# Optimization experiments

Hardware: AMD Instinct MI355X
Metric: run time of the kernel (lower is better)

## Reference

```python
import jax, jax.numpy as jnp
import numpy as np

N = 50000   # nodes
E = 800000  # edges (no self loops; conv adds them)
F = 64      # in_channels == out_channels
P = 6       # pos dim (pos_nn MLP input = 6)
H = 64      # hidden width of pos_nn / attn_nn


def _mlp(x, W1, b1, W2, b2):
    # PyG MLP([a, 64, b], norm=None, plain_last=False): ReLU after both layers
    return jax.nn.relu(jax.nn.relu(x @ W1 + b1) @ W2 + b2)


def setup_inputs() -> dict:
    key = jax.random.key(0)
    ks = jax.random.split(key, 16)

    def w(k, shape, fan_in):
        return jax.random.normal(k, shape, jnp.float32) / np.sqrt(fan_in)

    src = jax.random.randint(ks[0], (E,), 0, N)
    dst = jax.random.randint(ks[1], (E,), 0, N)
    src = jnp.where(src == dst, (src + 1) % N, src)  # no pre-existing self loops
    edge_index = jnp.stack([src, dst]).astype(jnp.int32)

    return dict(
        x=jax.random.normal(ks[2], (N, F), jnp.float32),
        pos=jax.random.normal(ks[3], (N, P), jnp.float32),
        edge_index=edge_index,
        W_in=w(ks[4], (F, F), F), b_in=jnp.zeros((F,), jnp.float32),
        W_out=w(ks[5], (F, F), F), b_out=jnp.zeros((F,), jnp.float32),
        W_lin=w(ks[6], (F, F), F),   # conv value proj, bias=False
        W_src=w(ks[7], (F, F), F),   # lin_src, bias=False
        W_dst=w(ks[8], (F, F), F),   # lin_dst, bias=False
        Wp1=w(ks[9], (P, H), P), bp1=jnp.zeros((H,), jnp.float32),
        Wp2=w(ks[10], (H, F), H), bp2=jnp.zeros((F,), jnp.float32),
        Wa1=w(ks[11], (F, H), F), ba1=jnp.zeros((H,), jnp.float32),
        Wa2=w(ks[12], (H, F), H), ba2=jnp.zeros((F,), jnp.float32),
    )


def reference(x, pos, edge_index, W_in, b_in, W_out, b_out, W_lin, W_src, W_dst,
              Wp1, bp1, Wp2, bp2, Wa1, ba1, Wa2, ba2):
    residual = jax.lax.stop_gradient(x)  # residual = x.clone().detach()
    h = jax.nn.relu(x @ W_in + b_in)

    # PointTransformerConv
    a_src = h @ W_src
    a_dst = h @ W_dst
    v = h @ W_lin

    loop = jnp.arange(N, dtype=edge_index.dtype)  # add_self_loops=True
    src = jnp.concatenate([edge_index[0], loop])
    dst = jnp.concatenate([edge_index[1], loop])

    delta = _mlp(pos[dst] - pos[src], Wp1, bp1, Wp2, bp2)        # pos_nn(pos_i - pos_j)
    alpha = _mlp(a_dst[dst] - a_src[src] + delta, Wa1, ba1, Wa2, ba2)

    # scatter-softmax over destination neighborhoods (per channel)
    m = jax.ops.segment_max(alpha, dst, num_segments=N)
    e = jnp.exp(alpha - m[dst])
    s = jax.ops.segment_sum(e, dst, num_segments=N)
    wgt = e / (s[dst] + 1e-16)

    msg = wgt * (v[src] + delta)
    out = jax.ops.segment_sum(msg, dst, num_segments=N)

    out = jax.nn.relu(out @ W_out + b_out)
    return out + residual
```

## Files before the change

### kernel.cpp

```cpp
#include <hip/hip_runtime.h>

#define NN 50000
#define NE 800000
#define ETOT (NE + NN)
#define NB ((NN + 255) / 256)

typedef _Float16 f16;
typedef _Float16 v8h __attribute__((ext_vector_type(8)));
typedef float v4f __attribute__((ext_vector_type(4)));

__device__ __forceinline__ float bcast(float v, int lane) {
  return __int_as_float(__builtin_amdgcn_readlane(__float_as_int(v), lane));
}

__device__ __forceinline__ int fr_off(int kb, int nb, int q, int p) {
  return (((nb * 2 + kb) * 4 + q) * 16 + p) * 8;
}


__global__ __launch_bounds__(256) void k_setup(
    const float* __restrict__ W_in, const float* __restrict__ W_src,
    const float* __restrict__ W_dst, const float* __restrict__ W_lin,
    const float* __restrict__ W_out, const float* __restrict__ Wp2,
    const float* __restrict__ Wa1, const float* __restrict__ Wa2,
    const float* __restrict__ Wp1, f16* __restrict__ FR,
    const int* __restrict__ edst, int* __restrict__ deg) {
  const int t = blockIdx.x * 256 + threadIdx.x;
  if (t < NE) atomicAdd(&deg[edst[t]], 1);
  if (t < 8 * 4096) {
    const float* Ws[8] = {W_in, W_src, W_dst, W_lin, W_out, Wp2, Wa1, Wa2};
    const int m = t >> 12, idx = t & 4095;
    const int i = idx & 7, p = (idx >> 3) & 15, q = (idx >> 7) & 3;
    const int kb = (idx >> 9) & 1, nb = (idx >> 10) & 3;
    FR[t] = (f16)Ws[m][(kb * 32 + q * 8 + i) * 64 + nb * 16 + p];
  } else if (t < 8 * 4096 + 2048) {
    const int idx = t - 8 * 4096;
    const int i = idx & 7, p = (idx >> 3) & 15, q = (idx >> 7) & 3, nb = idx >> 9;
    const int k = q * 8 + i;
    FR[t] = (k < 6) ? (f16)Wp1[k * 64 + nb * 16 + p] : (f16)0.f;
  }
}


__global__ __launch_bounds__(256) void k_scan1(const int* __restrict__ deg,
                                               int* __restrict__ bsum) {
  __shared__ int ws[4];
  const int t = threadIdx.x, b = blockIdx.x;
  const int i = b * 256 + t;
  int s = (i < NN) ? (deg[i] + 1) : 0;
#pragma unroll
  for (int d = 1; d < 64; d <<= 1) s += __shfl_xor(s, d, 64);
  if ((t & 63) == 0) ws[t >> 6] = s;
  __syncthreads();
  if (t == 0) bsum[b] = ws[0] + ws[1] + ws[2] + ws[3];
}

__global__ __launch_bounds__(256) void k_scan2(const int* __restrict__ bsum,
                                               int* __restrict__ bpre,
                                               int* __restrict__ offsets) {
  __shared__ int ws[4];
  const int t = threadIdx.x, lane = t & 63, w = t >> 6;
  int v = (t < NB) ? bsum[t] : 0;
  int x = v;
#pragma unroll
  for (int d = 1; d < 64; d <<= 1) {
    int y = __shfl_up(x, d, 64);
    if (lane >= d) x += y;
  }
  if (lane == 63) ws[w] = x;
  __syncthreads();
  if (t == 0) {
    int c = 0;
#pragma unroll
    for (int j = 0; j < 4; ++j) { int tmp = ws[j]; ws[j] = c; c += tmp; }
    offsets[NN] = c;
  }
  __syncthreads();
  if (t < NB) bpre[t] = ws[w] + x - v;
}

__global__ __launch_bounds__(256) void k_scan3(
    const int* __restrict__ deg, const int* __restrict__ bpre,
    int* __restrict__ offsets, int* __restrict__ ssrc, int* __restrict__ cursor) {
  __shared__ int ws[4], wpre[4];
  const int t = threadIdx.x, b = blockIdx.x, lane = t & 63, w = t >> 6;
  const int i = b * 256 + t;
  int v = (i < NN) ? (deg[i] + 1) : 0;
  int x = v;
#pragma unroll
  for (int d = 1; d < 64; d <<= 1) {
    int y = __shfl_up(x, d, 64);
    if (lane >= d) x += y;
  }
  if (lane == 63) ws[w] = x;
  __syncthreads();
  if (t == 0) {
    int c = 0;
#pragma unroll
    for (int j = 0; j < 4; ++j) { wpre[j] = c; c += ws[j]; }
  }
  __syncthreads();
  if (i < NN) {
    const int off = bpre[b] + wpre[w] + x - v;
    offsets[i] = off;
    ssrc[off] = i;
    cursor[i] = off + 1;
  }
}

__global__ void k_scatter(const int* __restrict__ src, const int* __restrict__ dst,
                          int* __restrict__ cursor, int* __restrict__ ssrc) {
  int e = blockIdx.x * 256 + threadIdx.x;
  if (e < NE) {
    int p = atomicAdd(&cursor[dst[e]], 1);
    ssrc[p] = src[e];
  }
}


__global__ __launch_bounds__(256, 2) void k_node(
    const float* __restrict__ x, const float* __restrict__ pos,
    const float* __restrict__ b_in, const f16* __restrict__ FR,
    f16* __restrict__ adsth, f16* __restrict__ vh,
    f16* __restrict__ asrch, f16* __restrict__ Qh) {
  __shared__ f16 lds[4][16 * 72];
  const int lane = threadIdx.x & 63, w = threadIdx.x >> 6;
  const int q = lane >> 4, p = lane & 15;
  const int base = (blockIdx.x * 4 + w) * 16;
  if (base >= NN) return;
  const f16* FWin = FR;
  const f16* FWsrc = FR + 1 * 4096;
  const f16* FWdst = FR + 2 * 4096;
  const f16* FWlin = FR + 3 * 4096;
  const f16* FWp1 = FR + 8 * 4096;

  v8h xa[2];
#pragma unroll
  for (int kb = 0; kb < 2; ++kb) {
    const float4 f0 = *(const float4*)(x + (base + p) * 64 + kb * 32 + q * 8);
    const float4 f1 = *(const float4*)(x + (base + p) * 64 + kb * 32 + q * 8 + 4);
    v8h a;
    a[0] = (f16)f0.x; a[1] = (f16)f0.y; a[2] = (f16)f0.z; a[3] = (f16)f0.w;
    a[4] = (f16)f1.x; a[5] = (f16)f1.y; a[6] = (f16)f1.z; a[7] = (f16)f1.w;
    xa[kb] = a;
  }
#pragma unroll
  for (int nb = 0; nb < 4; ++nb) {
    v4f c = {0.f, 0.f, 0.f, 0.f};
    c = __builtin_amdgcn_mfma_f32_16x16x32_f16(xa[0], *(const v8h*)&FWin[fr_off(0, nb, q, p)], c, 0, 0, 0);
    c = __builtin_amdgcn_mfma_f32_16x16x32_f16(xa[1], *(const v8h*)&FWin[fr_off(1, nb, q, p)], c, 0, 0, 0);
    const float bi = b_in[p + 16 * nb];
#pragma unroll
    for (int r = 0; r < 4; ++r)
      lds[w][(q * 4 + r) * 72 + p + 16 * nb] = (f16)fmaxf(c[r] + bi, 0.f);
  }
  v8h hA[2];
#pragma unroll
  for (int kb = 0; kb < 2; ++kb)
    hA[kb] = *(const v8h*)&lds[w][p * 72 + kb * 32 + q * 8];

#pragma unroll
  for (int nb = 0; nb < 4; ++nb) {
    v4f c = {0.f, 0.f, 0.f, 0.f};
    c = __builtin_amdgcn_mfma_f32_16x16x32_f16(hA[0], *(const v8h*)&FWsrc[fr_off(0, nb, q, p)], c, 0, 0, 0);
    c = __builtin_amdgcn_mfma_f32_16x16x32_f16(hA[1], *(const v8h*)&FWsrc[fr_off(1, nb, q, p)], c, 0, 0, 0);
#pragma unroll
    for (int r = 0; r < 4; ++r)
      asrch[(base + q * 4 + r) * 64 + p + 16 * nb] = (f16)c[r];
  }
#pragma unroll
  for (int nb = 0; nb < 4; ++nb) {
    v4f c = {0.f, 0.f, 0.f, 0.f};
    c = __builtin_amdgcn_mfma_f32_16x16x32_f16(hA[0], *(const v8h*)&FWdst[fr_off(0, nb, q, p)], c, 0, 0, 0);
    c = __builtin_amdgcn_mfma_f32_16x16x32_f16(hA[1], *(const v8h*)&FWdst[fr_off(1, nb, q, p)], c, 0, 0, 0);
#pragma unroll
    for (int r = 0; r < 4; ++r)
      adsth[(base + q * 4 + r) * 64 + p + 16 * nb] = (f16)c[r];
  }
#pragma unroll
  for (int nb = 0; nb < 4; ++nb) {
    v4f c = {0.f, 0.f, 0.f, 0.f};
    c = __builtin_amdgcn_mfma_f32_16x16x32_f16(hA[0], *(const v8h*)&FWlin[fr_off(0, nb, q, p)], c, 0, 0, 0);
    c = __builtin_amdgcn_mfma_f32_16x16x32_f16(hA[1], *(const v8h*)&FWlin[fr_off(1, nb, q, p)], c, 0, 0, 0);
#pragma unroll
    for (int r = 0; r < 4; ++r)
      vh[(base + q * 4 + r) * 64 + p + 16 * nb] = (f16)c[r];
  }
  v8h pa;
#pragma unroll
  for (int i = 0; i < 8; ++i) {
    const int k = q * 8 + i;
    pa[i] = (k < 6) ? (f16)pos[(base + p) * 6 + k] : (f16)0.f;
  }
#pragma unroll
  for (int nb = 0; nb < 4; ++nb) {
    const v8h b = *(const v8h*)&FWp1[(((nb * 4 + q) * 16) + p) * 8];
    v4f c = {0.f, 0.f, 0.f, 0.f};
    c = __builtin_amdgcn_mfma_f32_16x16x32_f16(pa, b, c, 0, 0, 0);
#pragma unroll
    for (int r = 0; r < 4; ++r)
      Qh[(base + q * 4 + r) * 64 + p + 16 * nb] = (f16)c[r];
  }
}


__global__ __launch_bounds__(512, 4) void k_conv(
    const f16* __restrict__ Qh, const float* __restrict__ bp1,
    const f16* __restrict__ FRconv,
    const float* __restrict__ bp2, const float* __restrict__ ba1,
    const float* __restrict__ ba2,
    const f16* __restrict__ asrch, const f16* __restrict__ adsth,
    const f16* __restrict__ vh,
    const int* __restrict__ offsets, const int* __restrict__ ssrc,
    const float* __restrict__ W_out, const float* __restrict__ b_out,
    const float* __restrict__ x, float* __restrict__ out) {
  __shared__ f16 wfr[12288];
  __shared__ f16 tbufD[8][16 * 72];
  __shared__ f16 tbufH[8][16 * 72];
  __shared__ f16 stashQ[8][64];
  __shared__ f16 stashA[8][64];
  __shared__ float bias[192];
  const int t = threadIdx.x;
#pragma unroll
  for (int it = 0; it < 3; ++it)
    *(uint4*)&wfr[(it * 512 + t) * 8] = *(const uint4*)&FRconv[(it * 512 + t) * 8];
  if (t < 192) bias[t] = (t < 64) ? bp2[t] : (t < 128 ? ba1[t - 64] : ba2[t - 128]);

  const int lane = t & 63, w = t >> 6;
  const int q = lane >> 4, p = lane & 15;
  const int n = blockIdx.x * 8 + w;

  stashQ[w][lane] = (f16)((float)Qh[n * 64 + lane] + bp1[lane]);
  stashA[w][lane] = adsth[n * 64 + lane];
  __syncthreads();

  const int e0 = __builtin_amdgcn_readfirstlane(offsets[n]);
  const int e1 = __builtin_amdgcn_readfirstlane(offsets[n + 1]);
  const int cnt = e1 - e0;

  float s_[4], ac_[4];
#pragma unroll
  for (int nb = 0; nb < 4; ++nb) { s_[nb] = 0.f; ac_[nb] = 0.f; }

  for (int cb = 0; cb < cnt; cb += 16) {
    const int jA = ssrc[e0 + min(cb + p, cnt - 1)];
    v8h qj[2], aj[2], vA[2];
#pragma unroll
    for (int kb = 0; kb < 2; ++kb) {
      qj[kb] = *(const v8h*)(Qh + jA * 64 + kb * 32 + q * 8);
      aj[kb] = *(const v8h*)(asrch + jA * 64 + kb * 32 + q * 8);
      vA[kb] = *(const v8h*)(vh + jA * 64 + kb * 32 + q * 8);
    }
    v8h uA[2];
#pragma unroll
    for (int kb = 0; kb < 2; ++kb) {
      const v8h qi = *(const v8h*)&stashQ[w][kb * 32 + q * 8];
      v8h a;
#pragma unroll
      for (int i = 0; i < 8; ++i) {
        const f16 d = qi[i] - qj[kb][i];
        a[i] = d > (f16)0 ? d : (f16)0;
      }
      uA[kb] = a;
    }
    unsigned z0;
    asm volatile("v_mov_b32 %0, 0" : "=v"(z0));
#pragma unroll
    for (int nb = 0; nb < 4; ++nb) {
      v4f c = {0.f, 0.f, 0.f, 0.f};
      c = __builtin_amdgcn_mfma_f32_16x16x32_f16(uA[0], *(const v8h*)&wfr[z0 + fr_off(0, nb, q, p)], c, 0, 0, 0);
      c = __builtin_amdgcn_mfma_f32_16x16x32_f16(uA[1], *(const v8h*)&wfr[z0 + fr_off(1, nb, q, p)], c, 0, 0, 0);
      const float bp2c = bias[p + 16 * nb];
#pragma unroll
      for (int r = 0; r < 4; ++r)
        tbufD[w][(q * 4 + r) * 72 + p + 16 * nb] = (f16)fmaxf(c[r] + bp2c, 0.f);
    }
#pragma unroll
    for (int kb = 0; kb < 2; ++kb) {
      const v8h adc = *(const v8h*)&stashA[w][kb * 32 + q * 8];
      const v8h dj = *(const v8h*)&tbufD[w][p * 72 + kb * 32 + q * 8];
      uA[kb] = (adc - aj[kb]) + dj;
    }
    unsigned z1;
    asm volatile("v_mov_b32 %0, 4096" : "=v"(z1));
#pragma unroll
    for (int nb = 0; nb < 4; ++nb) {
      v4f c = {0.f, 0.f, 0.f, 0.f};
      c = __builtin_amdgcn_mfma_f32_16x16x32_f16(uA[0], *(const v8h*)&wfr[z1 + fr_off(0, nb, q, p)], c, 0, 0, 0);
      c = __builtin_amdgcn_mfma_f32_16x16x32_f16(uA[1], *(const v8h*)&wfr[z1 + fr_off(1, nb, q, p)], c, 0, 0, 0);
      const float ba1c = bias[64 + p + 16 * nb];
#pragma unroll
      for (int r = 0; r < 4; ++r)
        tbufH[w][(q * 4 + r) * 72 + p + 16 * nb] = (f16)fmaxf(c[r] + ba1c, 0.f);
    }
#pragma unroll
    for (int kb = 0; kb < 2; ++kb)
      uA[kb] = *(const v8h*)&tbufH[w][p * 72 + kb * 32 + q * 8];
#pragma unroll
    for (int kb = 0; kb < 2; ++kb)
      *(v8h*)&tbufH[w][p * 72 + kb * 32 + q * 8] = vA[kb];
    unsigned z2;
    asm volatile("v_mov_b32 %0, 8192" : "=v"(z2));
#pragma unroll
    for (int nb = 0; nb < 4; ++nb) {
      v4f c = {0.f, 0.f, 0.f, 0.f};
      c = __builtin_amdgcn_mfma_f32_16x16x32_f16(uA[0], *(const v8h*)&wfr[z2 + fr_off(0, nb, q, p)], c, 0, 0, 0);
      c = __builtin_amdgcn_mfma_f32_16x16x32_f16(uA[1], *(const v8h*)&wfr[z2 + fr_off(1, nb, q, p)], c, 0, 0, 0);
      const float ba2c = bias[128 + p + 16 * nb];
#pragma unroll
      for (int r = 0; r < 4; ++r) {
        const bool ok = (cb + q * 4 + r) < cnt;
        const float al = ok ? fmaxf(c[r] + ba2c, 0.f) : -3.0e38f;
        const float wv = __expf(al);
        const float vj = (float)tbufH[w][(q * 4 + r) * 72 + p + 16 * nb];
        const float dC = (float)tbufD[w][(q * 4 + r) * 72 + p + 16 * nb];
        s_[nb] += wv;
        ac_[nb] = fmaf(wv, vj + dC, ac_[nb]);
      }
    }
  }
#pragma unroll
  for (int st = 16; st <= 32; st <<= 1) {
#pragma unroll
    for (int nb = 0; nb < 4; ++nb) {
      s_[nb] += __shfl_xor(s_[nb], st, 64);
      ac_[nb] += __shfl_xor(ac_[nb], st, 64);
    }
  }
  const float o = ac_[q] / (s_[q] + 1e-16f);
  float a0 = b_out[lane], a1 = 0.f, a2 = 0.f, a3 = 0.f;
#pragma unroll
  for (int k = 0; k < 64; k += 4) {
    a0 = fmaf(bcast(o, k + 0), W_out[(k + 0) * 64 + lane], a0);
    a1 = fmaf(bcast(o, k + 1), W_out[(k + 1) * 64 + lane], a1);
    a2 = fmaf(bcast(o, k + 2), W_out[(k + 2) * 64 + lane], a2);
    a3 = fmaf(bcast(o, k + 3), W_out[(k + 3) * 64 + lane], a3);
  }
  out[n * 64 + lane] = fmaxf((a0 + a1) + (a2 + a3), 0.f) + x[n * 64 + lane];
}


extern "C" void kernel_launch(void* const* d_in, const int* in_sizes, int n_in,
                              void* d_out, int out_size, void* d_ws, size_t ws_size,
                              hipStream_t stream) {
  const float* x     = (const float*)d_in[0];
  const float* pos   = (const float*)d_in[1];
  const int*   ei    = (const int*)d_in[2];
  const float* W_in  = (const float*)d_in[3];
  const float* b_in  = (const float*)d_in[4];
  const float* W_out = (const float*)d_in[5];
  const float* b_out = (const float*)d_in[6];
  const float* W_lin = (const float*)d_in[7];
  const float* W_src = (const float*)d_in[8];
  const float* W_dst = (const float*)d_in[9];
  const float* Wp1   = (const float*)d_in[10];
  const float* bp1   = (const float*)d_in[11];
  const float* Wp2   = (const float*)d_in[12];
  const float* bp2   = (const float*)d_in[13];
  const float* Wa1   = (const float*)d_in[14];
  const float* ba1   = (const float*)d_in[15];
  const float* Wa2   = (const float*)d_in[16];
  const float* ba2   = (const float*)d_in[17];

  f16*  Qh     = (f16*)d_ws;
  f16*  asrch  = Qh + NN * 64;
  f16*  adsth  = asrch + NN * 64;
  f16*  vh     = adsth + NN * 64;
  f16*  FR     = vh + NN * 64;
  int*  deg    = (int*)(FR + 8 * 4096 + 2048);
  int* offsets = deg + NN;
  int* cursor  = offsets + NN + 1;
  int* bsum    = cursor + NN;
  int* bpre    = bsum + NB;
  int* ssrc    = bpre + NB;

  const int* esrc = ei;
  const int* edst = ei + NE;

  hipMemsetAsync(deg, 0, NN * sizeof(int), stream);
  k_setup<<<(NE + 255) / 256, 256, 0, stream>>>(
      W_in, W_src, W_dst, W_lin, W_out, Wp2, Wa1, Wa2, Wp1, FR, edst, deg);
  k_node<<<(NN / 16 + 3) / 4, 256, 0, stream>>>(x, pos, b_in, FR, adsth, vh, asrch, Qh);
  k_scan1<<<NB, 256, 0, stream>>>(deg, bsum);
  k_scan2<<<1, 256, 0, stream>>>(bsum, bpre, offsets);
  k_scan3<<<NB, 256, 0, stream>>>(deg, bpre, offsets, ssrc, cursor);
  k_scatter<<<(NE + 255) / 256, 256, 0, stream>>>(esrc, edst, cursor, ssrc);
  k_conv<<<NN / 8, 512, 0, stream>>>(Qh, bp1, FR + 5 * 4096, bp2, ba1, ba2,
                                     asrch, adsth, vh, offsets, ssrc,
                                     W_out, b_out, x, (float*)d_out);
}
```

Baseline: 322.6 us.

## Merge scan kernels, share one LDS tile buffer, raise conv occupancy

The single-block scan2 kernel is removed; each scan3 block now reduces all block sums to get its own base offset, which saves one launch. In k_conv the two per-wave LDS transpose buffers become one, and the delta values are kept in registers for the final accumulation instead of being reread from LDS. Launch bounds rise from 4 to 6 blocks per CU, aiming for more resident waves. The catch is tighter register limits that may cause spills, and each scan block redundantly re-reducing the block sums.

After: 308.1 us. -4.5%, faster.

```diff
diff --git a/kernel.cpp b/kernel.cpp
--- a/kernel.cpp
+++ b/kernel.cpp
@@ -55,12 +55,28 @@
   if (t == 0) bsum[b] = ws[0] + ws[1] + ws[2] + ws[3];
 }
 
-__global__ __launch_bounds__(256) void k_scan2(const int* __restrict__ bsum,
-                                               int* __restrict__ bpre,
-                                               int* __restrict__ offsets) {
-  __shared__ int ws[4];
-  const int t = threadIdx.x, lane = t & 63, w = t >> 6;
-  int v = (t < NB) ? bsum[t] : 0;
+__global__ __launch_bounds__(256) void k_scan3(
+    const int* __restrict__ deg, const int* __restrict__ bsum,
+    int* __restrict__ offsets, int* __restrict__ ssrc, int* __restrict__ cursor) {
+  __shared__ int r1[4], r2[4], ws[4], wpre[4];
+  __shared__ int bbase;
+  const int t = threadIdx.x, b = blockIdx.x, lane = t & 63, w = t >> 6;
+  int bs = (t < NB) ? bsum[t] : 0;
+  int pr = (t < b) ? bs : 0;
+#pragma unroll
+  for (int d = 1; d < 64; d <<= 1) {
+    pr += __shfl_xor(pr, d, 64);
+    bs += __shfl_xor(bs, d, 64);
+  }
+  if (lane == 0) { r1[w] = pr; r2[w] = bs; }
+  __syncthreads();
+  if (t == 0) {
+    bbase = r1[0] + r1[1] + r1[2] + r1[3];
+    if (b == 0) offsets[NN] = r2[0] + r2[1] + r2[2] + r2[3];
+  }
+  __syncthreads();
+  const int i = b * 256 + t;
+  int v = (i < NN) ? (deg[i] + 1) : 0;
   int x = v;
 #pragma unroll
   for (int d = 1; d < 64; d <<= 1) {
@@ -72,36 +88,11 @@
   if (t == 0) {
     int c = 0;
 #pragma unroll
-    for (int j = 0; j < 4; ++j) { int tmp = ws[j]; ws[j] = c; c += tmp; }
-    offsets[NN] = c;
-  }
-  __syncthreads();
-  if (t < NB) bpre[t] = ws[w] + x - v;
-}
-
-__global__ __launch_bounds__(256) void k_scan3(
-    const int* __restrict__ deg, const int* __restrict__ bpre,
-    int* __restrict__ offsets, int* __restrict__ ssrc, int* __restrict__ cursor) {
-  __shared__ int ws[4], wpre[4];
-  const int t = threadIdx.x, b = blockIdx.x, lane = t & 63, w = t >> 6;
-  const int i = b * 256 + t;
-  int v = (i < NN) ? (deg[i] + 1) : 0;
-  int x = v;
-#pragma unroll
-  for (int d = 1; d < 64; d <<= 1) {
-    int y = __shfl_up(x, d, 64);
-    if (lane >= d) x += y;
-  }
-  if (lane == 63) ws[w] = x;
-  __syncthreads();
-  if (t == 0) {
-    int c = 0;
-#pragma unroll
     for (int j = 0; j < 4; ++j) { wpre[j] = c; c += ws[j]; }
   }
   __syncthreads();
   if (i < NN) {
-    const int off = bpre[b] + wpre[w] + x - v;
+    const int off = bbase + wpre[w] + x - v;
     offsets[i] = off;
     ssrc[off] = i;
     cursor[i] = off + 1;
@@ -204,7 +195,7 @@
 }
 
 
-__global__ __launch_bounds__(512, 4) void k_conv(
+__global__ __launch_bounds__(512, 6) void k_conv(
     const f16* __restrict__ Qh, const float* __restrict__ bp1,
     const f16* __restrict__ FRconv,
     const float* __restrict__ bp2, const float* __restrict__ ba1,
@@ -215,8 +206,7 @@
     const float* __restrict__ W_out, const float* __restrict__ b_out,
     const float* __restrict__ x, float* __restrict__ out) {
   __shared__ f16 wfr[12288];
-  __shared__ f16 tbufD[8][16 * 72];
-  __shared__ f16 tbufH[8][16 * 72];
+  __shared__ f16 tbuf[8][16 * 72];
   __shared__ f16 stashQ[8][64];
   __shared__ f16 stashA[8][64];
   __shared__ float bias[192];
@@ -265,6 +255,7 @@
     }
     unsigned z0;
     asm volatile("v_mov_b32 %0, 0" : "=v"(z0));
+    v8h dc0, dc1;
 #pragma unroll
     for (int nb = 0; nb < 4; ++nb) {
       v4f c = {0.f, 0.f, 0.f, 0.f};
@@ -272,13 +263,17 @@
       c = __builtin_amdgcn_mfma_f32_16x16x32_f16(uA[1], *(const v8h*)&wfr[z0 + fr_off(1, nb, q, p)], c, 0, 0, 0);
       const float bp2c = bias[p + 16 * nb];
 #pragma unroll
-      for (int r = 0; r < 4; ++r)
-        tbufD[w][(q * 4 + r) * 72 + p + 16 * nb] = (f16)fmaxf(c[r] + bp2c, 0.f);
+      for (int r = 0; r < 4; ++r) {
+        const f16 dh = (f16)fmaxf(c[r] + bp2c, 0.f);
+        tbuf[w][(q * 4 + r) * 72 + p + 16 * nb] = dh;
+        const int idx = nb * 4 + r;
+        if (idx < 8) dc0[idx] = dh; else dc1[idx - 8] = dh;
+      }
     }
 #pragma unroll
     for (int kb = 0; kb < 2; ++kb) {
       const v8h adc = *(const v8h*)&stashA[w][kb * 32 + q * 8];
-      const v8h dj = *(const v8h*)&tbufD[w][p * 72 + kb * 32 + q * 8];
+      const v8h dj = *(const v8h*)&tbuf[w][p * 72 + kb * 32 + q * 8];
       uA[kb] = (adc - aj[kb]) + dj;
     }
     unsigned z1;
@@ -291,14 +286,14 @@
       const float ba1c = bias[64 + p + 16 * nb];
 #pragma unroll
       for (int r = 0; r < 4; ++r)
-        tbufH[w][(q * 4 + r) * 72 + p + 16 * nb] = (f16)fmaxf(c[r] + ba1c, 0.f);
+        tbuf[w][(q * 4 + r) * 72 + p + 16 * nb] = (f16)fmaxf(c[r] + ba1c, 0.f);
     }
 #pragma unroll
     for (int kb = 0; kb < 2; ++kb)
-      uA[kb] = *(const v8h*)&tbufH[w][p * 72 + kb * 32 + q * 8];
+      uA[kb] = *(const v8h*)&tbuf[w][p * 72 + kb * 32 + q * 8];
 #pragma unroll
     for (int kb = 0; kb < 2; ++kb)
-      *(v8h*)&tbufH[w][p * 72 + kb * 32 + q * 8] = vA[kb];
+      *(v8h*)&tbuf[w][p * 72 + kb * 32 + q * 8] = vA[kb];
     unsigned z2;
     asm volatile("v_mov_b32 %0, 8192" : "=v"(z2));
 #pragma unroll
@@ -312,8 +307,9 @@
         const bool ok = (cb + q * 4 + r) < cnt;
         const float al = ok ? fmaxf(c[r] + ba2c, 0.f) : -3.0e38f;
         const float wv = __expf(al);
-        const float vj = (float)tbufH[w][(q * 4 + r) * 72 + p + 16 * nb];
-        const float dC = (float)tbufD[w][(q * 4 + r) * 72 + p + 16 * nb];
+        const float vj = (float)tbuf[w][(q * 4 + r) * 72 + p + 16 * nb];
+        const int idx = nb * 4 + r;
+        const float dC = (float)((idx < 8) ? dc0[idx] : dc1[idx - 8]);
         s_[nb] += wv;
         ac_[nb] = fmaf(wv, vj + dC, ac_[nb]);
       }
@@ -371,8 +367,7 @@
   int* offsets = deg + NN;
   int* cursor  = offsets + NN + 1;
   int* bsum    = cursor + NN;
-  int* bpre    = bsum + NB;
-  int* ssrc    = bpre + NB;
+  int* ssrc    = bsum + NB;
 
   const int* esrc = ei;
   const int* edst = ei + NE;
@@ -382,8 +377,7 @@
       W_in, W_src, W_dst, W_lin, W_out, Wp2, Wa1, Wa2, Wp1, FR, edst, deg);
   k_node<<<(NN / 16 + 3) / 4, 256, 0, stream>>>(x, pos, b_in, FR, adsth, vh, asrch, Qh);
   k_scan1<<<NB, 256, 0, stream>>>(deg, bsum);
-  k_scan2<<<1, 256, 0, stream>>>(bsum, bpre, offsets);
-  k_scan3<<<NB, 256, 0, stream>>>(deg, bpre, offsets, ssrc, cursor);
+  k_scan3<<<NB, 256, 0, stream>>>(deg, bsum, offsets, ssrc, cursor);
   k_scatter<<<(NE + 255) / 256, 256, 0, stream>>>(esrc, edst, cursor, ssrc);
   k_conv<<<NN / 8, 512, 0, stream>>>(Qh, bp1, FR + 5 * 4096, bp2, ba1, ba2,
                                      asrch, adsth, vh, offsets, ssrc,
```
